# Kernel optimization log

Hardware: AMD Instinct MI355X
Metric: run time of the kernel (lower is better)

Reference implementation:

```python
import jax, jax.numpy as jnp
import numpy as np

DIM = 768
HEADS = 16
HEAD_DIM = DIM // HEADS  # 48


def setup_inputs() -> dict:
    key = jax.random.key(0)
    ks = jax.random.split(key, 9)
    s = 1.0 / np.sqrt(DIM)
    inp = {
        "x": jax.random.normal(ks[0], (4, 2048, DIM), dtype=jnp.float32),
        "Wq": jax.random.uniform(ks[1], (DIM, DIM), jnp.float32, -s, s),
        "bq": jax.random.uniform(ks[2], (DIM,), jnp.float32, -s, s),
        "Wk": jax.random.uniform(ks[3], (DIM, DIM), jnp.float32, -s, s),
        "bk": jax.random.uniform(ks[4], (DIM,), jnp.float32, -s, s),
        "Wv": jax.random.uniform(ks[5], (DIM, DIM), jnp.float32, -s, s),
        "bv": jax.random.uniform(ks[6], (DIM,), jnp.float32, -s, s),
        "Wo": jax.random.uniform(ks[7], (DIM, DIM), jnp.float32, -s, s),
        "bo": jax.random.uniform(ks[8], (DIM,), jnp.float32, -s, s),
    }
    return inp


def reference(x, Wq, bq, Wk, bk, Wv, bv, Wo, bo):
    B, S, _ = x.shape
    # torch nn.Linear: y = x @ W.T + b
    q = x @ Wq.T + bq
    k = x @ Wk.T + bk
    v = x @ Wv.T + bv
    # split heads: (B, H, S, Dh)
    q = q.reshape(B, S, HEADS, HEAD_DIM).transpose(0, 2, 1, 3)
    k = k.reshape(B, S, HEADS, HEAD_DIM).transpose(0, 2, 1, 3)
    v = v.reshape(B, S, HEADS, HEAD_DIM).transpose(0, 2, 1, 3)
    score = jnp.einsum("bhqd,bhkd->bhqk", q, k) / jnp.sqrt(jnp.float32(HEAD_DIM))
    attn = jax.nn.softmax(score, axis=-1)
    out = jnp.einsum("bhqk,bhkd->bhqd", attn, v)
    out = out.transpose(0, 2, 1, 3).reshape(B, S, DIM)
    return out @ Wo.T + bo
```

## Files before the change

kernel.cpp:

```cpp
#include <hip/hip_runtime.h>

#define DIM 768
#define SEQ 2048
#define NB 4
#define NH 16
#define DH 48
#define DP 64
#define BHN (NB*NH)
#define MTOK (NB*SEQ)

typedef __attribute__((ext_vector_type(8))) short bf16x8;
typedef __attribute__((ext_vector_type(4))) float f32x4;
typedef __attribute__((ext_vector_type(4))) unsigned int u32x4;

__device__ __forceinline__ unsigned short f32_to_bf16(float f) {
    union { float f; unsigned int u; } v; v.f = f;
    unsigned int r = v.u + 0x7fff + ((v.u >> 16) & 1);
    return (unsigned short)(r >> 16);
}

#if __has_builtin(__builtin_amdgcn_exp2f)
#define EXP2F(x) __builtin_amdgcn_exp2f(x)
#else
#define EXP2F(x) exp2f(x)
#endif

#define GL_LDS16(g, l) __builtin_amdgcn_global_load_lds( \
    (const __attribute__((address_space(1))) void*)(g),  \
    (__attribute__((address_space(3))) void*)(l), 16, 0, 0)

__global__ void cvt_f32_bf16(const float* __restrict__ src, unsigned short* __restrict__ dst, int n) {
    int i = (blockIdx.x * blockDim.x + threadIdx.x) * 4;
    if (i + 3 < n) {
        const float4 v = *(const float4*)(src + i);
        ushort4 o;
        o.x = f32_to_bf16(v.x); o.y = f32_to_bf16(v.y);
        o.z = f32_to_bf16(v.z); o.w = f32_to_bf16(v.w);
        *(ushort4*)(dst + i) = o;
    }
}

__global__ void cvt4_f32_bf16(const float* __restrict__ a, const float* __restrict__ b,
                              const float* __restrict__ c, const float* __restrict__ d,
                              unsigned short* __restrict__ dst, int n_each) {
    const float* srcs[4] = {a, b, c, d};
    const float* src = srcs[blockIdx.y];
    unsigned short* out = dst + blockIdx.y * n_each;
    int i = (blockIdx.x * blockDim.x + threadIdx.x) * 4;
    if (i + 3 < n_each) {
        const float4 v = *(const float4*)(src + i);
        ushort4 o;
        o.x = f32_to_bf16(v.x); o.y = f32_to_bf16(v.y);
        o.z = f32_to_bf16(v.z); o.w = f32_to_bf16(v.w);
        *(ushort4*)(out + i) = o;
    }
}

#define BK 32

__global__ __launch_bounds__(256) void qkv_gemm(
    const unsigned short* __restrict__ xb,
    const unsigned short* __restrict__ wb,
    const float* __restrict__ bq, const float* __restrict__ bk, const float* __restrict__ bv,
    unsigned short* __restrict__ Qb, unsigned short* __restrict__ Kb, unsigned short* __restrict__ Vt)
{
    const int z = blockIdx.z;
    const unsigned short* W = wb + z * (DIM * DIM);
    const float* bias = (z == 0) ? bq : (z == 1) ? bk : bv;
    const int row0 = blockIdx.x * 128;
    const int col0 = blockIdx.y * 128;

    __shared__ __align__(16) short As[128 * BK];
    __shared__ __align__(16) short Bs[128 * BK];

    const int tid = threadIdx.x;
    const int lane = tid & 63;
    const int w = tid >> 6;
    const int wy = w >> 1, wx = w & 1;
    const int l15 = lane & 15, quad = lane >> 4;
    const int lr = lane >> 2;
    const int lco = (lane & 3) * 8;

    f32x4 acc[4][4];
    for (int mi = 0; mi < 4; ++mi) for (int ni = 0; ni < 4; ++ni)
        for (int r = 0; r < 4; ++r) acc[mi][ni][r] = 0.f;

    for (int kt = 0; kt < DIM / BK; ++kt) {
        #pragma unroll
        for (int j = 0; j < 2; ++j) {
            const int c = w * 2 + j;
            GL_LDS16(&xb[(row0 + c * 16 + lr) * DIM + kt * BK + lco], &As[c * 512]);
            GL_LDS16(&W [(col0 + c * 16 + lr) * DIM + kt * BK + lco], &Bs[c * 512]);
        }
        __syncthreads();
        bf16x8 af[4], bfr[4];
        #pragma unroll
        for (int mi = 0; mi < 4; ++mi)
            af[mi] = *(const bf16x8*)&As[(wy * 64 + mi * 16 + l15) * BK + quad * 8];
        #pragma unroll
        for (int ni = 0; ni < 4; ++ni)
            bfr[ni] = *(const bf16x8*)&Bs[(wx * 64 + ni * 16 + l15) * BK + quad * 8];
        #pragma unroll
        for (int mi = 0; mi < 4; ++mi)
            #pragma unroll
            for (int ni = 0; ni < 4; ++ni)
                acc[mi][ni] = __builtin_amdgcn_mfma_f32_16x16x32_bf16(af[mi], bfr[ni], acc[mi][ni], 0, 0, 0);
        __syncthreads();
    }

    const float qscale = 0.14433756729740643f * 1.4426950408889634f;

    if (z == 2) {
        #pragma unroll
        for (int mi = 0; mi < 4; ++mi) {
            #pragma unroll
            for (int ni = 0; ni < 4; ++ni) {
                int col = col0 + wx * 64 + ni * 16 + l15;
                int h = col / DH, d = col - h * DH;
                int row = row0 + wy * 64 + mi * 16 + quad * 4;
                int b = row >> 11, s = row & 2047;
                float bi = bias[col];
                union { ushort4 v; unsigned short e[4]; } pk;
                #pragma unroll
                for (int r = 0; r < 4; ++r)
                    pk.e[r] = f32_to_bf16(acc[mi][ni][r] + bi);
                *(ushort4*)&Vt[((b * NH + h) * DP + d) * SEQ + s] = pk.v;
            }
        }
    } else {
        #pragma unroll
        for (int mi = 0; mi < 4; ++mi) {
            #pragma unroll
            for (int ni = 0; ni < 4; ++ni) {
                #pragma unroll
                for (int r = 0; r < 4; ++r) {
                    int row = row0 + wy * 64 + mi * 16 + quad * 4 + r;
                    int col = col0 + wx * 64 + ni * 16 + l15;
                    float v = acc[mi][ni][r] + bias[col];
                    int b = row >> 11, s = row & 2047;
                    int h = col / DH, d = col - h * DH;
                    int bh = b * NH + h;
                    if (z == 0) Qb[(bh * SEQ + s) * DP + d] = f32_to_bf16(v * qscale);
                    else        Kb[(bh * SEQ + s) * DP + d] = f32_to_bf16(v);
                }
            }
        }
    }
}

__global__ __launch_bounds__(256) void out_gemm(
    const unsigned short* __restrict__ ab,
    const unsigned short* __restrict__ Wo,
    const float* __restrict__ bo,
    float* __restrict__ out)
{
    const int row0 = blockIdx.x * 128;
    const int col0 = blockIdx.y * 128;

    __shared__ __align__(16) short As[128 * BK];
    __shared__ __align__(16) short Bs[128 * BK];

    const int tid = threadIdx.x;
    const int lane = tid & 63;
    const int w = tid >> 6;
    const int wy = w >> 1, wx = w & 1;
    const int l15 = lane & 15, quad = lane >> 4;
    const int lr = lane >> 2;
    const int lco = (lane & 3) * 8;

    f32x4 acc[4][4];
    for (int mi = 0; mi < 4; ++mi) for (int ni = 0; ni < 4; ++ni)
        for (int r = 0; r < 4; ++r) acc[mi][ni][r] = 0.f;

    for (int kt = 0; kt < DIM / BK; ++kt) {
        #pragma unroll
        for (int j = 0; j < 2; ++j) {
            const int c = w * 2 + j;
            GL_LDS16(&ab[(row0 + c * 16 + lr) * DIM + kt * BK + lco], &As[c * 512]);
            GL_LDS16(&Wo[(col0 + c * 16 + lr) * DIM + kt * BK + lco], &Bs[c * 512]);
        }
        __syncthreads();
        bf16x8 af[4], bfr[4];
        #pragma unroll
        for (int mi = 0; mi < 4; ++mi)
            af[mi] = *(const bf16x8*)&As[(wy * 64 + mi * 16 + l15) * BK + quad * 8];
        #pragma unroll
        for (int ni = 0; ni < 4; ++ni)
            bfr[ni] = *(const bf16x8*)&Bs[(wx * 64 + ni * 16 + l15) * BK + quad * 8];
        #pragma unroll
        for (int mi = 0; mi < 4; ++mi)
            #pragma unroll
            for (int ni = 0; ni < 4; ++ni)
                acc[mi][ni] = __builtin_amdgcn_mfma_f32_16x16x32_bf16(af[mi], bfr[ni], acc[mi][ni], 0, 0, 0);
        __syncthreads();
    }

    #pragma unroll
    for (int mi = 0; mi < 4; ++mi)
        #pragma unroll
        for (int ni = 0; ni < 4; ++ni)
            #pragma unroll
            for (int r = 0; r < 4; ++r) {
                int row = row0 + wy * 64 + mi * 16 + quad * 4 + r;
                int col = col0 + wx * 64 + ni * 16 + l15;
                out[row * DIM + col] = acc[mi][ni][r] + bo[col];
            }
}

__device__ __forceinline__ int keyperm(int a) {
    return (a & 32) + ((a & 12) << 1) + ((a & 16) >> 2) + (a & 3);
}

__global__ __launch_bounds__(256, 2) void attn_kernel(
    const unsigned short* __restrict__ Qb,
    const unsigned short* __restrict__ Kb,
    const unsigned short* __restrict__ Vt,
    unsigned short* __restrict__ Ob)
{
    const int bh = blockIdx.x;
    const int tile = blockIdx.y;
    const int tid = threadIdx.x;
    const int w = tid >> 6;
    const int lane = tid & 63;
    const int l15 = lane & 15, quad = lane >> 4;

    const unsigned short* Qh = Qb + bh * SEQ * DP;
    const unsigned short* Kh = Kb + bh * SEQ * DP;
    const unsigned short* Vh = Vt + bh * DP * SEQ;
    const int q0 = tile * 256 + w * 64;

    __shared__ __align__(16) short Ks[64 * 64];
    __shared__ __align__(16) short Vs[48 * 64];

    bf16x8 aq[4][2];
    #pragma unroll
    for (int m = 0; m < 4; ++m)
        #pragma unroll
        for (int ks = 0; ks < 2; ++ks)
            aq[m][ks] = *(const bf16x8*)&Qh[(q0 + m * 16 + l15) * DP + ks * 32 + quad * 8];
    if (quad >= 2) {
        const bf16x8 z8 = {0, 0, 0, 0, 0, 0, 0, 0};
        #pragma unroll
        for (int m = 0; m < 4; ++m) aq[m][1] = z8;
    }

    f32x4 o[4][3];
    #pragma unroll
    for (int m = 0; m < 4; ++m) for (int ni = 0; ni < 3; ++ni)
        for (int r = 0; r < 4; ++r) o[m][ni][r] = 0.f;
    float ls[4][2];
    #pragma unroll
    for (int m = 0; m < 4; ++m) { ls[m][0] = 0.f; ls[m][1] = 0.f; }

    const f32x4 FZ = {0.f, 0.f, 0.f, 0.f};

    const int ra = tid >> 2;
    const int pc = tid & 3;
    const int lcA = ((pc ^ (ra & 7)) * 8);
    const int lcB = (((pc + 4) ^ (ra & 7)) * 8);
    const int kaR = keyperm(ra);
    const int ldsA = ra * 64 + pc * 8;
    const int ldsB = ra * 64 + (pc + 4) * 8;
    const bool vld = (tid < 192);

    bf16x8 kr0, kr1, vr0, vr1;
    kr0 = *(const bf16x8*)&Kh[kaR * DP + lcA];
    kr1 = *(const bf16x8*)&Kh[kaR * DP + lcB];
    if (vld) {
        vr0 = *(const bf16x8*)&Vh[ra * SEQ + lcA];
        vr1 = *(const bf16x8*)&Vh[ra * SEQ + lcB];
    }

    for (int kt = 0; kt < SEQ / 64; ++kt) {
        __syncthreads();
        *(bf16x8*)&Ks[ldsA] = kr0;
        *(bf16x8*)&Ks[ldsB] = kr1;
        if (vld) {
            *(bf16x8*)&Vs[ldsA] = vr0;
            *(bf16x8*)&Vs[ldsB] = vr1;
        }
        if (kt + 1 < SEQ / 64) {
            const int k0n = (kt + 1) * 64;
            kr0 = *(const bf16x8*)&Kh[(k0n + kaR) * DP + lcA];
            kr1 = *(const bf16x8*)&Kh[(k0n + kaR) * DP + lcB];
            if (vld) {
                vr0 = *(const bf16x8*)&Vh[ra * SEQ + k0n + lcA];
                vr1 = *(const bf16x8*)&Vh[ra * SEQ + k0n + lcB];
            }
        }
        __syncthreads();

        bf16x8 ak0[4], ak1[4];
        #pragma unroll
        for (int n = 0; n < 4; ++n) {
            ak0[n] = *(const bf16x8*)&Ks[(n * 16 + l15) * 64 + ((quad ^ (l15 & 7)) * 8)];
            ak1[n] = *(const bf16x8*)&Ks[(n * 16 + l15) * 64 + (((4 + quad) ^ (l15 & 7)) * 8)];
        }
        bf16x8 av[2][3];
        #pragma unroll
        for (int ks = 0; ks < 2; ++ks)
            #pragma unroll
            for (int mt = 0; mt < 3; ++mt)
                av[ks][mt] = *(const bf16x8*)&Vs[(mt * 16 + l15) * 64 + (((ks * 4 + quad) ^ (l15 & 7)) * 8)];

        #pragma unroll
        for (int mp = 0; mp < 2; ++mp) {
            const int m0 = 2 * mp, m1 = 2 * mp + 1;
            f32x4 sc[2][4];
            #pragma unroll
            for (int n = 0; n < 4; ++n) {
                sc[0][n] = __builtin_amdgcn_mfma_f32_16x16x32_bf16(ak0[n], aq[m0][0], FZ, 0, 0, 0);
                sc[1][n] = __builtin_amdgcn_mfma_f32_16x16x32_bf16(ak0[n], aq[m1][0], FZ, 0, 0, 0);
            }
            #pragma unroll
            for (int n = 0; n < 4; ++n) {
                sc[0][n] = __builtin_amdgcn_mfma_f32_16x16x32_bf16(ak1[n], aq[m0][1], sc[0][n], 0, 0, 0);
                sc[1][n] = __builtin_amdgcn_mfma_f32_16x16x32_bf16(ak1[n], aq[m1][1], sc[1][n], 0, 0, 0);
            }
            union { u32x4 u; bf16x8 h; } bp[2][2];
            #pragma unroll
            for (int mi = 0; mi < 2; ++mi) {
                #pragma unroll
                for (int ks = 0; ks < 2; ++ks) {
                    #pragma unroll
                    for (int w2 = 0; w2 < 4; ++w2) {
                        const int j0 = 2 * w2, j1 = 2 * w2 + 1;
                        float p0 = EXP2F(sc[mi][2 * ks + (j0 >> 2)][j0 & 3]);
                        float p1 = EXP2F(sc[mi][2 * ks + (j1 >> 2)][j1 & 3]);
                        ls[2 * mp + mi][w2 & 1] += (p0 + p1);
                        bp[mi][ks].u[w2] = __builtin_amdgcn_perm(__float_as_uint(p1), __float_as_uint(p0), 0x07060302u);
                    }
                }
            }
            #pragma unroll
            for (int ks = 0; ks < 2; ++ks)
                #pragma unroll
                for (int mt = 0; mt < 3; ++mt) {
                    o[m0][mt] = __builtin_amdgcn_mfma_f32_16x16x32_bf16(av[ks][mt], bp[0][ks].h, o[m0][mt], 0, 0, 0);
                    o[m1][mt] = __builtin_amdgcn_mfma_f32_16x16x32_bf16(av[ks][mt], bp[1][ks].h, o[m1][mt], 0, 0, 0);
                }
        }
    }

    const int b = bh >> 4, h = bh & 15;
    #pragma unroll
    for (int m = 0; m < 4; ++m) {
        float lsum = ls[m][0] + ls[m][1];
        lsum += __shfl_xor(lsum, 16);
        lsum += __shfl_xor(lsum, 32);
        float inv = 1.f / lsum;
        #pragma unroll
        for (int mt = 0; mt < 3; ++mt)
            #pragma unroll
            for (int r = 0; r < 4; ++r) {
                int token = b * SEQ + q0 + m * 16 + l15;
                int d = mt * 16 + quad * 4 + r;
                Ob[token * DIM + h * DH + d] = f32_to_bf16(o[m][mt][r] * inv);
            }
    }
}

extern "C" void kernel_launch(void* const* d_in, const int* in_sizes, int n_in,
                              void* d_out, int out_size, void* d_ws, size_t ws_size,
                              hipStream_t stream) {
    const float* x  = (const float*)d_in[0];
    const float* Wq = (const float*)d_in[1]; const float* bq = (const float*)d_in[2];
    const float* Wk = (const float*)d_in[3]; const float* bk = (const float*)d_in[4];
    const float* Wv = (const float*)d_in[5]; const float* bv = (const float*)d_in[6];
    const float* Wo = (const float*)d_in[7]; const float* bo = (const float*)d_in[8];

    unsigned char* ws = (unsigned char*)d_ws;
    unsigned short* xb = (unsigned short*)(ws);
    unsigned short* wb = (unsigned short*)(ws + 12582912);
    unsigned short* Qb = (unsigned short*)(ws + 17301504);
    unsigned short* Kb = (unsigned short*)(ws + 34078720);
    unsigned short* Vt = (unsigned short*)(ws + 50855936);
    unsigned short* Ob = (unsigned short*)(ws + 67633152);

    cvt_f32_bf16<<<6144, 256, 0, stream>>>(x, xb, MTOK * DIM);
    cvt4_f32_bf16<<<dim3(576, 4), 256, 0, stream>>>(Wq, Wk, Wv, Wo, wb, DIM * DIM);

    qkv_gemm<<<dim3(MTOK / 128, DIM / 128, 3), 256, 0, stream>>>(xb, wb, bq, bk, bv, Qb, Kb, Vt);
    attn_kernel<<<dim3(BHN, SEQ / 256), 256, 0, stream>>>(Qb, Kb, Vt, Ob);
    out_gemm<<<dim3(MTOK / 128, DIM / 128), 256, 0, stream>>>(Ob, wb + 3 * DIM * DIM, bo, (float*)d_out);
}
```

Baseline: 218.2 us.

## Merge conversion kernels, vectorize Q/K epilogue stores, recoalesce attention K/V loads

Merges the x and weight fp32-to-bf16 conversions into one launch. For the Q and K outputs, the GEMM swaps the MFMA operands so each lane holds four consecutive feature columns, which allows a float4 bias load and packed ushort4 stores in place of scalar 2-byte scatters. The attention kernel's K/V global-to-register staging is remapped so eight lanes cover a full 64-element row, giving more contiguous global accesses. These changes target launch overhead and poorly coalesced stores and loads, at the cost of some added index arithmetic.

```diff
diff --git a/kernel.cpp b/kernel.cpp
--- a/kernel.cpp
+++ b/kernel.cpp
@@ -29,31 +29,27 @@
     (const __attribute__((address_space(1))) void*)(g),  \
     (__attribute__((address_space(3))) void*)(l), 16, 0, 0)
 
-__global__ void cvt_f32_bf16(const float* __restrict__ src, unsigned short* __restrict__ dst, int n) {
+__global__ void cvt_all(const float* __restrict__ x,
+                        const float* __restrict__ Wq, const float* __restrict__ Wk,
+                        const float* __restrict__ Wv, const float* __restrict__ Wo,
+                        unsigned short* __restrict__ xb, unsigned short* __restrict__ wb) {
+    const int nx = MTOK * DIM;
+    const int nw = DIM * DIM;
     int i = (blockIdx.x * blockDim.x + threadIdx.x) * 4;
-    if (i + 3 < n) {
-        const float4 v = *(const float4*)(src + i);
-        ushort4 o;
-        o.x = f32_to_bf16(v.x); o.y = f32_to_bf16(v.y);
-        o.z = f32_to_bf16(v.z); o.w = f32_to_bf16(v.w);
-        *(ushort4*)(dst + i) = o;
-    }
-}
-
-__global__ void cvt4_f32_bf16(const float* __restrict__ a, const float* __restrict__ b,
-                              const float* __restrict__ c, const float* __restrict__ d,
-                              unsigned short* __restrict__ dst, int n_each) {
-    const float* srcs[4] = {a, b, c, d};
-    const float* src = srcs[blockIdx.y];
-    unsigned short* out = dst + blockIdx.y * n_each;
-    int i = (blockIdx.x * blockDim.x + threadIdx.x) * 4;
-    if (i + 3 < n_each) {
-        const float4 v = *(const float4*)(src + i);
-        ushort4 o;
-        o.x = f32_to_bf16(v.x); o.y = f32_to_bf16(v.y);
-        o.z = f32_to_bf16(v.z); o.w = f32_to_bf16(v.w);
-        *(ushort4*)(out + i) = o;
-    }
+    const float* src; unsigned short* dst; int off;
+    if (i < nx) { src = x; dst = xb; off = i; }
+    else {
+        int j = i - nx;
+        int r = j / nw;
+        off = j - r * nw;
+        src = (r == 0) ? Wq : (r == 1) ? Wk : (r == 2) ? Wv : Wo;
+        dst = wb + r * nw;
+    }
+    const float4 v = *(const float4*)(src + off);
+    ushort4 o;
+    o.x = f32_to_bf16(v.x); o.y = f32_to_bf16(v.y);
+    o.z = f32_to_bf16(v.z); o.w = f32_to_bf16(v.w);
+    *(ushort4*)(dst + off) = o;
 }
 
 #define BK 32
@@ -100,11 +96,19 @@
         #pragma unroll
         for (int ni = 0; ni < 4; ++ni)
             bfr[ni] = *(const bf16x8*)&Bs[(wx * 64 + ni * 16 + l15) * BK + quad * 8];
-        #pragma unroll
-        for (int mi = 0; mi < 4; ++mi)
-            #pragma unroll
-            for (int ni = 0; ni < 4; ++ni)
-                acc[mi][ni] = __builtin_amdgcn_mfma_f32_16x16x32_bf16(af[mi], bfr[ni], acc[mi][ni], 0, 0, 0);
+        if (z == 2) {
+            #pragma unroll
+            for (int mi = 0; mi < 4; ++mi)
+                #pragma unroll
+                for (int ni = 0; ni < 4; ++ni)
+                    acc[mi][ni] = __builtin_amdgcn_mfma_f32_16x16x32_bf16(af[mi], bfr[ni], acc[mi][ni], 0, 0, 0);
+        } else {
+            #pragma unroll
+            for (int mi = 0; mi < 4; ++mi)
+                #pragma unroll
+                for (int ni = 0; ni < 4; ++ni)
+                    acc[mi][ni] = __builtin_amdgcn_mfma_f32_16x16x32_bf16(bfr[ni], af[mi], acc[mi][ni], 0, 0, 0);
+        }
         __syncthreads();
     }
 
@@ -128,21 +132,30 @@
             }
         }
     } else {
+        unsigned short* dst = (z == 0) ? Qb : Kb;
         #pragma unroll
         for (int mi = 0; mi < 4; ++mi) {
+            int token = row0 + wy * 64 + mi * 16 + l15;
+            int b = token >> 11, s = token & 2047;
             #pragma unroll
             for (int ni = 0; ni < 4; ++ni) {
-                #pragma unroll
-                for (int r = 0; r < 4; ++r) {
-                    int row = row0 + wy * 64 + mi * 16 + quad * 4 + r;
-                    int col = col0 + wx * 64 + ni * 16 + l15;
-                    float v = acc[mi][ni][r] + bias[col];
-                    int b = row >> 11, s = row & 2047;
-                    int h = col / DH, d = col - h * DH;
-                    int bh = b * NH + h;
-                    if (z == 0) Qb[(bh * SEQ + s) * DP + d] = f32_to_bf16(v * qscale);
-                    else        Kb[(bh * SEQ + s) * DP + d] = f32_to_bf16(v);
+                int f0 = col0 + wx * 64 + ni * 16 + quad * 4;
+                const float4 b4 = *(const float4*)&bias[f0];
+                int h = f0 / DH, d0 = f0 - h * DH;
+                int bh = b * NH + h;
+                union { ushort4 v; unsigned short e[4]; } pk;
+                if (z == 0) {
+                    pk.e[0] = f32_to_bf16((acc[mi][ni][0] + b4.x) * qscale);
+                    pk.e[1] = f32_to_bf16((acc[mi][ni][1] + b4.y) * qscale);
+                    pk.e[2] = f32_to_bf16((acc[mi][ni][2] + b4.z) * qscale);
+                    pk.e[3] = f32_to_bf16((acc[mi][ni][3] + b4.w) * qscale);
+                } else {
+                    pk.e[0] = f32_to_bf16(acc[mi][ni][0] + b4.x);
+                    pk.e[1] = f32_to_bf16(acc[mi][ni][1] + b4.y);
+                    pk.e[2] = f32_to_bf16(acc[mi][ni][2] + b4.z);
+                    pk.e[3] = f32_to_bf16(acc[mi][ni][3] + b4.w);
                 }
+                *(ushort4*)&dst[(bh * SEQ + s) * DP + d0] = pk.v;
             }
         }
     }
@@ -254,39 +267,32 @@
 
     const f32x4 FZ = {0.f, 0.f, 0.f, 0.f};
 
-    const int ra = tid >> 2;
-    const int pc = tid & 3;
-    const int lcA = ((pc ^ (ra & 7)) * 8);
-    const int lcB = (((pc + 4) ^ (ra & 7)) * 8);
-    const int kaR = keyperm(ra);
-    const int ldsA = ra * 64 + pc * 8;
-    const int ldsB = ra * 64 + (pc + 4) * 8;
-    const bool vld = (tid < 192);
+    const int sa = tid >> 3;
+    const int sc_ = tid & 7;
+    const int lc8 = (sc_ ^ (sa & 7)) * 8;
+    const int ka0 = keyperm(sa), ka1 = keyperm(sa + 32);
+    const int lds_w0 = sa * 64 + sc_ * 8;
+    const int lds_w1 = (sa + 32) * 64 + sc_ * 8;
+    const bool vsec = (tid < 128);
 
     bf16x8 kr0, kr1, vr0, vr1;
-    kr0 = *(const bf16x8*)&Kh[kaR * DP + lcA];
-    kr1 = *(const bf16x8*)&Kh[kaR * DP + lcB];
-    if (vld) {
-        vr0 = *(const bf16x8*)&Vh[ra * SEQ + lcA];
-        vr1 = *(const bf16x8*)&Vh[ra * SEQ + lcB];
-    }
+    kr0 = *(const bf16x8*)&Kh[ka0 * DP + lc8];
+    kr1 = *(const bf16x8*)&Kh[ka1 * DP + lc8];
+    vr0 = *(const bf16x8*)&Vh[sa * SEQ + lc8];
+    if (vsec) vr1 = *(const bf16x8*)&Vh[(sa + 32) * SEQ + lc8];
 
     for (int kt = 0; kt < SEQ / 64; ++kt) {
         __syncthreads();
-        *(bf16x8*)&Ks[ldsA] = kr0;
-        *(bf16x8*)&Ks[ldsB] = kr1;
-        if (vld) {
-            *(bf16x8*)&Vs[ldsA] = vr0;
-            *(bf16x8*)&Vs[ldsB] = vr1;
-        }
+        *(bf16x8*)&Ks[lds_w0] = kr0;
+        *(bf16x8*)&Ks[lds_w1] = kr1;
+        *(bf16x8*)&Vs[lds_w0] = vr0;
+        if (vsec) *(bf16x8*)&Vs[lds_w1] = vr1;
         if (kt + 1 < SEQ / 64) {
             const int k0n = (kt + 1) * 64;
-            kr0 = *(const bf16x8*)&Kh[(k0n + kaR) * DP + lcA];
-            kr1 = *(const bf16x8*)&Kh[(k0n + kaR) * DP + lcB];
-            if (vld) {
-                vr0 = *(const bf16x8*)&Vh[ra * SEQ + k0n + lcA];
-                vr1 = *(const bf16x8*)&Vh[ra * SEQ + k0n + lcB];
-            }
+            kr0 = *(const bf16x8*)&Kh[(k0n + ka0) * DP + lc8];
+            kr1 = *(const bf16x8*)&Kh[(k0n + ka1) * DP + lc8];
+            vr0 = *(const bf16x8*)&Vh[sa * SEQ + k0n + lc8];
+            if (vsec) vr1 = *(const bf16x8*)&Vh[(sa + 32) * SEQ + k0n + lc8];
         }
         __syncthreads();
 
@@ -377,8 +383,7 @@
     unsigned short* Vt = (unsigned short*)(ws + 50855936);
     unsigned short* Ob = (unsigned short*)(ws + 67633152);
 
-    cvt_f32_bf16<<<6144, 256, 0, stream>>>(x, xb, MTOK * DIM);
-    cvt4_f32_bf16<<<dim3(576, 4), 256, 0, stream>>>(Wq, Wk, Wv, Wo, wb, DIM * DIM);
+    cvt_all<<<8448, 256, 0, stream>>>(x, Wq, Wk, Wv, Wo, xb, wb);
 
     qkv_gemm<<<dim3(MTOK / 128, DIM / 128, 3), 256, 0, stream>>>(xb, wb, bq, bk, bv, Qb, Kb, Vt);
     attn_kernel<<<dim3(BHN, SEQ / 256), 256, 0, stream>>>(Qb, Kb, Vt, Ob);
```

Measured after the change: 241.6 us. 1.11x slower.
